# Kernel optimization log

Hardware: AMD Instinct MI355X
Metric: run time of the kernel (lower is better)

Reference implementation:

```python
import jax, jax.numpy as jnp
import numpy as np

RESO = 128

def _prefix_a3(layer, off0):
    # a3[0]=off0; a3[i]=a3[i-1]+2*layer[i-1]+2*layer[i]
    t = jnp.concatenate([jnp.zeros((1,), layer.dtype), 2.0 * layer[:-1] + 2.0 * layer[1:]])
    return off0 + jnp.cumsum(t)

def _prefix_a6(layer, a3):
    # a6[0]=0; a6[i]=a6[i-1]+3*layer[i-1]+layer[i]+2*a3[i-1]
    s = jnp.concatenate([jnp.zeros((1,), layer.dtype), 3.0 * layer[:-1] + layer[1:] + 2.0 * a3[:-1]])
    return jnp.cumsum(s)

def _decode(idx, reso):
    iz = idx % reso                 # selects xLayer channels (0,3)
    iy = (idx // reso) % reso       # selects yLayer channels (1,4)
    ix = idx // (reso * reso)       # selects zLayer channels (2,5)
    return ix, iy, iz

def setup_inputs() -> dict:
    key = jax.random.key(0)
    k1, k2, k3, k4 = jax.random.split(key, 4)
    N = 4194304
    reso = RESO
    ncells = reso ** 3
    renderPointList = jax.random.normal(k1, (N, 3), dtype=jnp.float32) * reso * 0.3 + reso * 0.5
    sdfPointList = jax.random.normal(k2, (N, 3), dtype=jnp.float32) * reso * 0.3 + reso * 0.5
    renderIndexList = jax.random.randint(k3, (N,), 0, ncells, dtype=jnp.int64) if jax.config.jax_enable_x64 else jax.random.randint(k3, (N,), 0, ncells).astype(jnp.int32)
    sdfIndexList = jax.random.randint(k4, (N,), 0, ncells).astype(renderIndexList.dtype)
    xLayer = jnp.ones((reso,), dtype=jnp.float32)
    yLayer = jnp.ones((reso,), dtype=jnp.float32)
    zLayer = jnp.ones((reso,), dtype=jnp.float32)
    c = 1.0 - reso
    offset = jnp.array([2 * c, 2 * c, 2 * c, 3 * c * c - float(reso) ** 2], dtype=jnp.float32)
    return {"renderPointList": renderPointList, "renderIndexList": renderIndexList,
            "sdfPointList": sdfPointList, "sdfIndexList": sdfIndexList,
            "xLayer": xLayer, "yLayer": yLayer, "zLayer": zLayer, "offset": offset}

def reference(renderPointList, renderIndexList, sdfPointList, sdfIndexList, xLayer, yLayer, zLayer, offset):
    reso = xLayer.shape[0]
    xA3 = _prefix_a3(xLayer, offset[0])
    yA4 = _prefix_a3(yLayer, offset[1])
    zA5 = _prefix_a3(zLayer, offset[2])
    xA6 = _prefix_a6(xLayer, xA3)
    yA6 = _prefix_a6(yLayer, yA4)
    zA6 = _prefix_a6(zLayer, zA5)

    # ---- SDF evaluation ----
    ix, iy, iz = _decode(sdfIndexList, reso)
    px, py, pz = sdfPointList[:, 0], sdfPointList[:, 1], sdfPointList[:, 2]
    a0 = xLayer[iz] * px
    a1 = yLayer[iy] * py
    a2 = zLayer[ix] * pz
    a3 = xA3[iz]
    a4 = yA4[iy]
    a5 = zA5[ix]
    a6 = offset[3] + xA6[iz] + yA6[iy] + zA6[ix]
    num = (a0 + a3) * px + (a1 + a4) * py + (a2 + a5) * pz + a6
    den = jnp.sqrt((2 * a0 + a3) ** 2 + (2 * a1 + a4) ** 2 + (2 * a2 + a5) ** 2)
    sdfList = num / den / reso

    # ---- Normal evaluation ----
    jx, jy, jz = _decode(renderIndexList, reso)
    rx, ry, rz = renderPointList[:, 0], renderPointList[:, 1], renderPointList[:, 2]
    nx = 2 * xLayer[jz] * rx + xA3[jz]
    ny = 2 * yLayer[jy] * ry + yA4[jy]
    nz = 2 * zLayer[jx] * rz + zA5[jx]
    n = jnp.stack([nx, ny, nz], axis=1)  # [N,3]
    norm = jnp.sqrt(jnp.sum(n * n, axis=1, keepdims=True))
    normalList = n / jnp.maximum(norm, 1e-12)
    return (sdfList, normalList)
```

## Files before the change

kernel.cpp:

```cpp
#include <hip/hip_runtime.h>

#define RESO 128

__global__ __launch_bounds__(128) void scan_kernel(
    const float* __restrict__ xL, const float* __restrict__ yL,
    const float* __restrict__ zL, const float* __restrict__ off,
    float* __restrict__ ws)
{
    __shared__ float s_tmp[4];
    __shared__ float s_a3[RESO];

    const int tid  = threadIdx.x;
    const int lane = tid & 63;
    const int wave = tid >> 6;

    for (int ax = 0; ax < 3; ++ax) {
        const float* L = (ax == 0) ? xL : (ax == 1) ? yL : zL;
        const float li   = L[tid];
        const float lim1 = (tid > 0) ? L[tid - 1] : 0.f;

        float v = (tid == 0) ? 0.f : 2.f * lim1 + 2.f * li;
        #pragma unroll
        for (int o = 1; o < 64; o <<= 1) {
            float u = __shfl_up(v, o, 64);
            if (lane >= o) v += u;
        }
        if (lane == 63) s_tmp[wave] = v;
        __syncthreads();
        if (wave == 1) v += s_tmp[0];
        const float a3v = off[ax] + v;
        s_a3[tid] = a3v;
        __syncthreads();

        const float a3m1 = (tid > 0) ? s_a3[tid - 1] : 0.f;
        float w = (tid == 0) ? 0.f : 3.f * lim1 + li + 2.f * a3m1;
        #pragma unroll
        for (int o = 1; o < 64; o <<= 1) {
            float u = __shfl_up(w, o, 64);
            if (lane >= o) w += u;
        }
        if (lane == 63) s_tmp[2 + wave] = w;
        __syncthreads();
        if (wave == 1) w += s_tmp[2];

        ws[ax * RESO + tid]       = li;
        ws[(3 + ax) * RESO + tid] = a3v;
        ws[(6 + ax) * RESO + tid] = w;
        __syncthreads();
    }
}

__global__ __launch_bounds__(256) void fused_kernel(
    const float* __restrict__ renderPts, const int* __restrict__ renderIdx,
    const float* __restrict__ sdfPts,    const int* __restrict__ sdfIdx,
    const float* __restrict__ ws,        const float* __restrict__ off,
    float* __restrict__ sdfOut, float* __restrict__ nrmOut, int N)
{
    __shared__ float4 tab[3][RESO];

    const int tid = threadIdx.x;
    if (tid < RESO) {
        #pragma unroll
        for (int ax = 0; ax < 3; ++ax)
            tab[ax][tid] = make_float4(ws[ax * RESO + tid],
                                       ws[(3 + ax) * RESO + tid],
                                       ws[(6 + ax) * RESO + tid], 0.f);
    }
    __syncthreads();

    const int i = blockIdx.x * blockDim.x + tid;
    if (i >= N) return;

    const float off3 = off[3];

    const int sid = sdfIdx[i];
    const float px = sdfPts[3 * i + 0];
    const float py = sdfPts[3 * i + 1];
    const float pz = sdfPts[3 * i + 2];
    const float4 tx = tab[0][sid & 127];
    const float4 ty = tab[1][(sid >> 7) & 127];
    const float4 tz = tab[2][(sid >> 14) & 127];

    const float a0 = tx.x * px;
    const float a1 = ty.x * py;
    const float a2 = tz.x * pz;
    const float a6 = off3 + tx.z + ty.z + tz.z;
    const float num = (a0 + tx.y) * px + (a1 + ty.y) * py + (a2 + tz.y) * pz + a6;
    const float dx = 2.f * a0 + tx.y;
    const float dy = 2.f * a1 + ty.y;
    const float dz = 2.f * a2 + tz.y;
    const float d2 = dx * dx + dy * dy + dz * dz;
    sdfOut[i] = num * __builtin_amdgcn_rsqf(d2) * (1.0f / (float)RESO);

    const int rid = renderIdx[i];
    const float rx = renderPts[3 * i + 0];
    const float ry = renderPts[3 * i + 1];
    const float rz = renderPts[3 * i + 2];
    const float4 ux = tab[0][rid & 127];
    const float4 uy = tab[1][(rid >> 7) & 127];
    const float4 uz = tab[2][(rid >> 14) & 127];

    const float x = 2.f * ux.x * rx + ux.y;
    const float y = 2.f * uy.x * ry + uy.y;
    const float z = 2.f * uz.x * rz + uz.y;
    const float n2 = x * x + y * y + z * z;
    const float inv = __builtin_amdgcn_rsqf(fmaxf(n2, 1e-24f));
    nrmOut[3 * i + 0] = x * inv;
    nrmOut[3 * i + 1] = y * inv;
    nrmOut[3 * i + 2] = z * inv;
}

extern "C" void kernel_launch(void* const* d_in, const int* in_sizes, int n_in,
                              void* d_out, int out_size, void* d_ws, size_t ws_size,
                              hipStream_t stream)
{
    const float* renderPts = (const float*)d_in[0];
    const int*   renderIdx = (const int*)d_in[1];
    const float* sdfPts    = (const float*)d_in[2];
    const int*   sdfIdx    = (const int*)d_in[3];
    const float* xL        = (const float*)d_in[4];
    const float* yL        = (const float*)d_in[5];
    const float* zL        = (const float*)d_in[6];
    const float* off       = (const float*)d_in[7];

    float* ws  = (float*)d_ws;
    float* out = (float*)d_out;
    const int N = in_sizes[1];

    scan_kernel<<<1, 128, 0, stream>>>(xL, yL, zL, off, ws);

    const int block = 256;
    const int grid = (N + block - 1) / block;
    fused_kernel<<<grid, block, 0, stream>>>(renderPts, renderIdx, sdfPts, sdfIdx,
                                             ws, off, out, out + N, N);
}
```

Measured before the change: 187.5 us.

## Use persistent grid-stride loop with register prefetch of next element

```diff
diff --git a/kernel.cpp b/kernel.cpp
--- a/kernel.cpp
+++ b/kernel.cpp
@@ -54,60 +54,89 @@
     const float* __restrict__ renderPts, const int* __restrict__ renderIdx,
     const float* __restrict__ sdfPts,    const int* __restrict__ sdfIdx,
     const float* __restrict__ ws,        const float* __restrict__ off,
-    float* __restrict__ sdfOut, float* __restrict__ nrmOut, int N)
+    float* __restrict__ sdfOut, float* __restrict__ nrmOut, int N, int iters)
 {
-    __shared__ float4 tab[3][RESO];
+    __shared__ float4 tabS[3][RESO];
+    __shared__ float2 tabR[3][RESO];
 
     const int tid = threadIdx.x;
     if (tid < RESO) {
         #pragma unroll
-        for (int ax = 0; ax < 3; ++ax)
-            tab[ax][tid] = make_float4(ws[ax * RESO + tid],
-                                       ws[(3 + ax) * RESO + tid],
-                                       ws[(6 + ax) * RESO + tid], 0.f);
+        for (int ax = 0; ax < 3; ++ax) {
+            const float L  = ws[ax * RESO + tid];
+            const float a3 = ws[(3 + ax) * RESO + tid];
+            const float a6 = ws[(6 + ax) * RESO + tid];
+            tabS[ax][tid] = make_float4(L, a3, a6, 0.f);
+            tabR[ax][tid] = make_float2(L, a3);
+        }
     }
     __syncthreads();
 
-    const int i = blockIdx.x * blockDim.x + tid;
-    if (i >= N) return;
+    const float off3   = off[3];
+    const int   stride = gridDim.x * blockDim.x;
+    int t = blockIdx.x * blockDim.x + tid;
 
-    const float off3 = off[3];
+    int   sidA = 0, ridA = 0;
+    float spxA = 0.f, spyA = 0.f, spzA = 0.f;
+    float rpxA = 0.f, rpyA = 0.f, rpzA = 0.f;
+    if (t < N) {
+        sidA = sdfIdx[t];
+        const float* sp = &sdfPts[3 * t];
+        spxA = sp[0]; spyA = sp[1]; spzA = sp[2];
+        ridA = renderIdx[t];
+        const float* rp = &renderPts[3 * t];
+        rpxA = rp[0]; rpyA = rp[1]; rpzA = rp[2];
+    }
 
-    const int sid = sdfIdx[i];
-    const float px = sdfPts[3 * i + 0];
-    const float py = sdfPts[3 * i + 1];
-    const float pz = sdfPts[3 * i + 2];
-    const float4 tx = tab[0][sid & 127];
-    const float4 ty = tab[1][(sid >> 7) & 127];
-    const float4 tz = tab[2][(sid >> 14) & 127];
+    for (int it = 0; it < iters; ++it) {
+        const int tn = t + stride;
+        const bool more = (it + 1 < iters) && (tn < N);
 
-    const float a0 = tx.x * px;
-    const float a1 = ty.x * py;
-    const float a2 = tz.x * pz;
-    const float a6 = off3 + tx.z + ty.z + tz.z;
-    const float num = (a0 + tx.y) * px + (a1 + ty.y) * py + (a2 + tz.y) * pz + a6;
-    const float dx = 2.f * a0 + tx.y;
-    const float dy = 2.f * a1 + ty.y;
-    const float dz = 2.f * a2 + tz.y;
-    const float d2 = dx * dx + dy * dy + dz * dz;
-    sdfOut[i] = num * __builtin_amdgcn_rsqf(d2) * (1.0f / (float)RESO);
+        int   sidB = 0, ridB = 0;
+        float spxB = 0.f, spyB = 0.f, spzB = 0.f;
+        float rpxB = 0.f, rpyB = 0.f, rpzB = 0.f;
+        if (more) {
+            sidB = sdfIdx[tn];
+            const float* sp = &sdfPts[3 * tn];
+            spxB = sp[0]; spyB = sp[1]; spzB = sp[2];
+            ridB = renderIdx[tn];
+            const float* rp = &renderPts[3 * tn];
+            rpxB = rp[0]; rpyB = rp[1]; rpzB = rp[2];
+        }
 
-    const int rid = renderIdx[i];
-    const float rx = renderPts[3 * i + 0];
-    const float ry = renderPts[3 * i + 1];
-    const float rz = renderPts[3 * i + 2];
-    const float4 ux = tab[0][rid & 127];
-    const float4 uy = tab[1][(rid >> 7) & 127];
-    const float4 uz = tab[2][(rid >> 14) & 127];
+        if (t < N) {
+            const float4 tx = tabS[0][sidA & 127];
+            const float4 ty = tabS[1][(sidA >> 7) & 127];
+            const float4 tz = tabS[2][(sidA >> 14) & 127];
+            const float a0 = tx.x * spxA;
+            const float a1 = ty.x * spyA;
+            const float a2 = tz.x * spzA;
+            const float a6 = off3 + tx.z + ty.z + tz.z;
+            const float num = (a0 + tx.y) * spxA + (a1 + ty.y) * spyA
+                            + (a2 + tz.y) * spzA + a6;
+            const float dx = 2.f * a0 + tx.y;
+            const float dy = 2.f * a1 + ty.y;
+            const float dz = 2.f * a2 + tz.y;
+            const float d2 = dx * dx + dy * dy + dz * dz;
+            sdfOut[t] = num * __builtin_amdgcn_rsqf(d2) * (1.0f / (float)RESO);
 
-    const float x = 2.f * ux.x * rx + ux.y;
-    const float y = 2.f * uy.x * ry + uy.y;
-    const float z = 2.f * uz.x * rz + uz.y;
-    const float n2 = x * x + y * y + z * z;
-    const float inv = __builtin_amdgcn_rsqf(fmaxf(n2, 1e-24f));
-    nrmOut[3 * i + 0] = x * inv;
-    nrmOut[3 * i + 1] = y * inv;
-    nrmOut[3 * i + 2] = z * inv;
+            const float2 ux = tabR[0][ridA & 127];
+            const float2 uy = tabR[1][(ridA >> 7) & 127];
+            const float2 uz = tabR[2][(ridA >> 14) & 127];
+            const float x = 2.f * ux.x * rpxA + ux.y;
+            const float y = 2.f * uy.x * rpyA + uy.y;
+            const float z = 2.f * uz.x * rpzA + uz.y;
+            const float n2 = x * x + y * y + z * z;
+            const float inv = __builtin_amdgcn_rsqf(fmaxf(n2, 1e-24f));
+            float* no = &nrmOut[3 * t];
+            no[0] = x * inv; no[1] = y * inv; no[2] = z * inv;
+        }
+
+        sidA = sidB; ridA = ridB;
+        spxA = spxB; spyA = spyB; spzA = spzB;
+        rpxA = rpxB; rpyA = rpyB; rpzA = rpzB;
+        t = tn;
+    }
 }
 
 extern "C" void kernel_launch(void* const* d_in, const int* in_sizes, int n_in,
@@ -130,7 +159,10 @@
     scan_kernel<<<1, 128, 0, stream>>>(xL, yL, zL, off, ws);
 
     const int block = 256;
-    const int grid = (N + block - 1) / block;
+    const int grid  = 4096;
+    const int total_threads = grid * block;
+    const int iters = (N + total_threads - 1) / total_threads;
+
     fused_kernel<<<grid, block, 0, stream>>>(renderPts, renderIdx, sdfPts, sdfIdx,
-                                             ws, off, out, out + N, N);
+                                             ws, off, out, out + N, N, iters);
 }
```

Result: no change. 190.8 us (+1.8%).
